# Kernel optimization log

Measured on AMD Instinct MI355X. Metric: run time of the kernel, lower is better.

## Reference

```python
import jax, jax.numpy as jnp
import numpy as np

EMBED = 1024
HIDDEN = 4 * EMBED
EPS = 1e-5

def _layer_norm(x, g, b):
    mu = jnp.mean(x, axis=-1, keepdims=True)
    var = jnp.mean((x - mu) ** 2, axis=-1, keepdims=True)
    return (x - mu) * jax.lax.rsqrt(var + EPS) * g + b

def setup_inputs() -> dict:
    key = jax.random.key(0)
    ks = jax.random.split(key, 8)
    s = 1.0 / np.sqrt(EMBED)
    inp = {
        "x": jax.random.normal(ks[0], (4, 2048, EMBED), dtype=jnp.float32),
        "Wq": jax.random.normal(ks[1], (EMBED, EMBED), dtype=jnp.float32) * s,
        "bq": jnp.zeros((EMBED,), jnp.float32),
        "Wk": jax.random.normal(ks[2], (EMBED, EMBED), dtype=jnp.float32) * s,
        "bk": jnp.zeros((EMBED,), jnp.float32),
        "Wv": jax.random.normal(ks[3], (EMBED, EMBED), dtype=jnp.float32) * s,
        "bv": jnp.zeros((EMBED,), jnp.float32),
        "W1": jax.random.normal(ks[4], (EMBED, HIDDEN), dtype=jnp.float32) * s,
        "b1": jnp.zeros((HIDDEN,), jnp.float32),
        "W2": jax.random.normal(ks[5], (HIDDEN, EMBED), dtype=jnp.float32) * (1.0 / np.sqrt(HIDDEN)),
        "b2": jnp.zeros((EMBED,), jnp.float32),
        "g1": jnp.ones((EMBED,), jnp.float32),
        "be1": jnp.zeros((EMBED,), jnp.float32),
        "g2": jnp.ones((EMBED,), jnp.float32),
        "be2": jnp.zeros((EMBED,), jnp.float32),
    }
    return inp

def reference(x, Wq, bq, Wk, bk, Wv, bv, W1, b1, W2, b2, g1, be1, g2, be2):
    # pre-norm attention
    h = _layer_norm(x, g1, be1)
    Q = h @ Wq + bq  # [B,S,D]
    K = h @ Wk + bk
    V = h @ Wv + bv
    scale = 1.0 / jnp.sqrt(jnp.asarray(EMBED, x.dtype))
    scores = jnp.einsum('bqd,bkd->bqk', Q, K) * scale  # [B,S,S]
    weights = jax.nn.softmax(scores, axis=-1)
    attn = jnp.einsum('bqk,bkd->bqd', weights, V)
    x = x + attn
    # pre-norm MLP
    h2 = _layer_norm(x, g2, be2)
    ff = jax.nn.relu(h2 @ W1 + b1) @ W2 + b2
    return x + ff
```

## Files before the change

### kernel.cpp

```cpp
#include <hip/hip_runtime.h>

#define EMBED 1024
#define HID   4096
#define NB    4
#define SEQ   2048

typedef __attribute__((ext_vector_type(8)))  __bf16 bf16x8;
typedef __attribute__((ext_vector_type(4)))  float  f32x4;
typedef __attribute__((ext_vector_type(4)))  int    i32x4;
typedef unsigned short u16;

__device__ __forceinline__ u16 f2bf(float f) {
  unsigned u = __float_as_uint(f);
  u += 0x7FFFu + ((u >> 16) & 1u);
  return (u16)(u >> 16);
}
__device__ __forceinline__ float bf2f(u16 u) {
  return __uint_as_float(((unsigned)u) << 16);
}

typedef const __attribute__((address_space(1))) unsigned int* gas_t;
typedef __attribute__((address_space(3))) unsigned int* las_t;
__device__ __forceinline__ void gld16(const void* g, void* l) {
  __builtin_amdgcn_global_load_lds((gas_t)g, (las_t)l, 16, 0, 0);
}

#define RD16(p)       __builtin_bit_cast(bf16x8, *(const i32x4*)(p))
#define MFMA16(a,b,c) __builtin_amdgcn_mfma_f32_16x16x32_bf16(a, b, c, 0, 0, 0)
#define SCHED0()      __builtin_amdgcn_sched_barrier(0)
#define BARR()        __builtin_amdgcn_s_barrier()
#define VMW(n)        asm volatile("s_waitcnt vmcnt(" #n ")" ::: "memory")

template<int EPI>
__global__ __launch_bounds__(512, 2) void gemm256v3(
    const u16* __restrict__ A, int lda, long long astr,
    const u16* __restrict__ B, int ldb, long long bstr,
    void* __restrict__ C, int ldc, long long cstr,
    const float* __restrict__ bias,
    float scale, int Kdim)
{
  __shared__ char lds[131072];

  const int tid  = threadIdx.x;
  const int lane = tid & 63;
  const int w    = tid >> 6;
  const int wr   = w >> 2, wc = w & 3;
  const int l15  = lane & 15, l4 = lane >> 4;

  const int gx   = gridDim.x;
  const int nwg  = gx * gridDim.y;
  const int orig = blockIdx.y * gx + blockIdx.x;
  const int t    = ((nwg & 7) == 0) ? ((orig & 7) * (nwg >> 3) + (orig >> 3)) : orig;
  const int bx   = t % gx, by = t / gx;

  const u16* Ab = A + (size_t)blockIdx.z * astr + (size_t)by * 256 * lda;
  const u16* Bb = B + (size_t)blockIdx.z * bstr + (size_t)bx * 256 * ldb;

  const int    srow = tid >> 3;
  const size_t sa   = (size_t)srow * lda + (size_t)(((tid & 7) ^ (srow & 7)) * 8);
  const size_t sb   = (size_t)srow * ldb + (size_t)(((tid & 7) ^ (srow & 7)) * 8);
  const int    ldst = tid * 16;

  auto stA = [&](int buf, int q, int kk) {
    gld16(Ab + (size_t)(q * 64) * lda + kk + sa, lds + buf * 65536 + q * 8192 + ldst);
  };
  auto stB = [&](int buf, int i, int kk) {
    gld16(Bb + (size_t)(i * 64) * ldb + kk + sb, lds + buf * 65536 + 32768 + i * 8192 + ldst);
  };

  const int arow = (wr * 128 + l15) * 128;
  const int brow = 32768 + (wc * 64 + l15) * 128;
  const int cp0  = ((0 + l4) ^ (l15 & 7)) * 16;
  const int cp1  = ((4 + l4) ^ (l15 & 7)) * 16;

  f32x4 acc[8][4] = {};
  const int NT = Kdim >> 6;

  stB(0, 0, 0); stB(0, 1, 0); stB(0, 2, 0); stB(0, 3, 0);
  stA(0, 0, 0); stA(0, 1, 0); stA(0, 2, 0); stA(0, 3, 0);

  for (int T = 0; T < NT; ++T) {
    const char* LB = lds + (T & 1) * 65536;
    VMW(0);
    SCHED0();
    BARR();
    SCHED0();

    if (T + 1 < NT) {
      const int b = (T & 1) ^ 1, kk = (T + 1) * 64;
      stB(b, 0, kk); stB(b, 1, kk); stB(b, 2, kk); stB(b, 3, kk);
      stA(b, 0, kk); stA(b, 1, kk); stA(b, 2, kk); stA(b, 3, kk);
    }

    bf16x8 b0 = RD16(LB + brow + 0 * 2048 + cp0);
    bf16x8 b1 = RD16(LB + brow + 1 * 2048 + cp0);
    bf16x8 b2 = RD16(LB + brow + 2 * 2048 + cp0);
    bf16x8 b3 = RD16(LB + brow + 3 * 2048 + cp0);
    bf16x8 b4 = RD16(LB + brow + 0 * 2048 + cp1);
    bf16x8 b5 = RD16(LB + brow + 1 * 2048 + cp1);
    bf16x8 b6 = RD16(LB + brow + 2 * 2048 + cp1);
    bf16x8 b7 = RD16(LB + brow + 3 * 2048 + cp1);

#define AQ(MP, x0, x1, x2, x3) \
    bf16x8 x0 = RD16(LB + arow + (MP) * 4096 + cp0); \
    bf16x8 x1 = RD16(LB + arow + (MP) * 4096 + cp1); \
    bf16x8 x2 = RD16(LB + arow + (MP) * 4096 + 2048 + cp0); \
    bf16x8 x3 = RD16(LB + arow + (MP) * 4096 + 2048 + cp1);

#define MQ(MP, x0, x1, x2, x3) \
    acc[2*(MP)  ][0] = MFMA16(x0, b0, acc[2*(MP)  ][0]); \
    acc[2*(MP)  ][1] = MFMA16(x0, b1, acc[2*(MP)  ][1]); \
    acc[2*(MP)  ][2] = MFMA16(x0, b2, acc[2*(MP)  ][2]); \
    acc[2*(MP)  ][3] = MFMA16(x0, b3, acc[2*(MP)  ][3]); \
    acc[2*(MP)+1][0] = MFMA16(x2, b0, acc[2*(MP)+1][0]); \
    acc[2*(MP)+1][1] = MFMA16(x2, b1, acc[2*(MP)+1][1]); \
    acc[2*(MP)+1][2] = MFMA16(x2, b2, acc[2*(MP)+1][2]); \
    acc[2*(MP)+1][3] = MFMA16(x2, b3, acc[2*(MP)+1][3]); \
    acc[2*(MP)  ][0] = MFMA16(x1, b4, acc[2*(MP)  ][0]); \
    acc[2*(MP)  ][1] = MFMA16(x1, b5, acc[2*(MP)  ][1]); \
    acc[2*(MP)  ][2] = MFMA16(x1, b6, acc[2*(MP)  ][2]); \
    acc[2*(MP)  ][3] = MFMA16(x1, b7, acc[2*(MP)  ][3]); \
    acc[2*(MP)+1][0] = MFMA16(x3, b4, acc[2*(MP)+1][0]); \
    acc[2*(MP)+1][1] = MFMA16(x3, b5, acc[2*(MP)+1][1]); \
    acc[2*(MP)+1][2] = MFMA16(x3, b6, acc[2*(MP)+1][2]); \
    acc[2*(MP)+1][3] = MFMA16(x3, b7, acc[2*(MP)+1][3]);

    AQ(0, a00, a01, a02, a03)
    AQ(1, a10, a11, a12, a13)
    MQ(0, a00, a01, a02, a03)
    AQ(2, a20, a21, a22, a23)
    MQ(1, a10, a11, a12, a13)
    AQ(3, a30, a31, a32, a33)
    MQ(2, a20, a21, a22, a23)
    MQ(3, a30, a31, a32, a33)
#undef AQ
#undef MQ
  }

  const int bm0 = by * 256 + wr * 128;
  const int bn0 = bx * 256 + wc * 64;
  u16* Ch = (u16*)C;
  #pragma unroll
  for (int mi = 0; mi < 8; ++mi) {
    #pragma unroll
    for (int ni = 0; ni < 4; ++ni) {
      const int col = bn0 + ni * 16 + l15;
      const int r0  = bm0 + mi * 16 + l4 * 4;
      float bv = 0.f;
      if (EPI == 0 || EPI == 3) bv = bias[col];
      #pragma unroll
      for (int r = 0; r < 4; ++r) {
        const size_t idx = (size_t)blockIdx.z * cstr + (size_t)(r0 + r) * ldc + col;
        const float v = acc[mi][ni][r];
        if      (EPI == 0) Ch[idx] = f2bf(v + bv);
        else if (EPI == 3) Ch[idx] = f2bf(fmaxf(v + bv, 0.f));
        else if (EPI == 6) Ch[idx] = f2bf(v * scale);
      }
    }
  }
}

template<int EPI>
__global__ __launch_bounds__(512, 2) void gemm128v3(
    const u16* __restrict__ A, int lda, long long astr,
    const u16* __restrict__ B, int ldb, long long bstr,
    void* __restrict__ C, int ldc, long long cstr,
    const float* __restrict__ bias,
    const void* __restrict__ add,
    float scale, int Kdim)
{
  __shared__ char lds[147456];
  const int SLOT = 49152;

  const int tid  = threadIdx.x;
  const int lane = tid & 63;
  const int w    = tid >> 6;
  const int wr   = w >> 1, wc = w & 1;
  const int l15  = lane & 15, l4 = lane >> 4;

  const int gx   = gridDim.x;
  const int nwg  = gx * gridDim.y;
  const int orig = blockIdx.y * gx + blockIdx.x;
  const int t    = ((nwg & 7) == 0) ? ((orig & 7) * (nwg >> 3) + (orig >> 3)) : orig;
  const int bx   = t % gx, by = t / gx;

  const u16* Ab = A + (size_t)blockIdx.z * astr + (size_t)by * 256 * lda;
  const u16* Bb = B + (size_t)blockIdx.z * bstr + (size_t)bx * 128 * ldb;

  size_t gaoff[4], gboff[2];
  #pragma unroll
  for (int i = 0; i < 4; ++i) {
    const int idx = i * 512 + tid, row = idx >> 3, gc = (idx & 7) ^ (row & 7);
    gaoff[i] = (size_t)row * lda + gc * 8;
  }
  #pragma unroll
  for (int j = 0; j < 2; ++j) {
    const int idx = j * 512 + tid, row = idx >> 3, gc = (idx & 7) ^ (row & 7);
    gboff[j] = (size_t)row * ldb + gc * 8;
  }

  auto stage = [&](char* SB, int kk) {
    #pragma unroll
    for (int i = 0; i < 4; ++i) gld16(Ab + gaoff[i] + kk, SB + (i * 512 + w * 64) * 16);
    #pragma unroll
    for (int j = 0; j < 2; ++j) gld16(Bb + gboff[j] + kk, SB + 32768 + (j * 512 + w * 64) * 16);
  };

  int aoff[4], boff[4];
  #pragma unroll
  for (int m = 0; m < 4; ++m) aoff[m] = (wr * 64 + m * 16 + l15) * 128;
  #pragma unroll
  for (int n = 0; n < 4; ++n) boff[n] = 32768 + (wc * 64 + n * 16 + l15) * 128;
  const int cp0 = ((0 + l4) ^ (l15 & 7)) * 16;
  const int cp1 = ((4 + l4) ^ (l15 & 7)) * 16;

  f32x4 acc[4][4] = {};
  const int NT = Kdim >> 6;

  stage(lds, 0);
  stage(lds + SLOT, 64);

  int sr = 0;
  for (int T = 0; T < NT; ++T) {
    const char* LB = lds + sr * SLOT;
    if (T == NT - 1) VMW(0);
    else             VMW(6);
    SCHED0();
    BARR();
    SCHED0();

    if (T + 2 < NT) stage(lds + ((sr + 2 >= 3) ? sr - 1 : sr + 2) * SLOT, (T + 2) * 64);

    bf16x8 b00 = RD16(LB + boff[0] + cp0);
    bf16x8 b01 = RD16(LB + boff[1] + cp0);
    bf16x8 b02 = RD16(LB + boff[2] + cp0);
    bf16x8 b03 = RD16(LB + boff[3] + cp0);
    bf16x8 b10 = RD16(LB + boff[0] + cp1);
    bf16x8 b11 = RD16(LB + boff[1] + cp1);
    bf16x8 b12 = RD16(LB + boff[2] + cp1);
    bf16x8 b13 = RD16(LB + boff[3] + cp1);
    bf16x8 a00 = RD16(LB + aoff[0] + cp0);
    bf16x8 a10 = RD16(LB + aoff[1] + cp0);
    bf16x8 a20 = RD16(LB + aoff[2] + cp0);
    bf16x8 a30 = RD16(LB + aoff[3] + cp0);
    bf16x8 a01 = RD16(LB + aoff[0] + cp1);
    bf16x8 a11 = RD16(LB + aoff[1] + cp1);
    bf16x8 a21 = RD16(LB + aoff[2] + cp1);
    bf16x8 a31 = RD16(LB + aoff[3] + cp1);

    acc[0][0] = MFMA16(a00, b00, acc[0][0]);
    acc[0][1] = MFMA16(a00, b01, acc[0][1]);
    acc[0][2] = MFMA16(a00, b02, acc[0][2]);
    acc[0][3] = MFMA16(a00, b03, acc[0][3]);
    acc[1][0] = MFMA16(a10, b00, acc[1][0]);
    acc[1][1] = MFMA16(a10, b01, acc[1][1]);
    acc[1][2] = MFMA16(a10, b02, acc[1][2]);
    acc[1][3] = MFMA16(a10, b03, acc[1][3]);
    acc[2][0] = MFMA16(a20, b00, acc[2][0]);
    acc[2][1] = MFMA16(a20, b01, acc[2][1]);
    acc[2][2] = MFMA16(a20, b02, acc[2][2]);
    acc[2][3] = MFMA16(a20, b03, acc[2][3]);
    acc[3][0] = MFMA16(a30, b00, acc[3][0]);
    acc[3][1] = MFMA16(a30, b01, acc[3][1]);
    acc[3][2] = MFMA16(a30, b02, acc[3][2]);
    acc[3][3] = MFMA16(a30, b03, acc[3][3]);
    acc[0][0] = MFMA16(a01, b10, acc[0][0]);
    acc[0][1] = MFMA16(a01, b11, acc[0][1]);
    acc[0][2] = MFMA16(a01, b12, acc[0][2]);
    acc[0][3] = MFMA16(a01, b13, acc[0][3]);
    acc[1][0] = MFMA16(a11, b10, acc[1][0]);
    acc[1][1] = MFMA16(a11, b11, acc[1][1]);
    acc[1][2] = MFMA16(a11, b12, acc[1][2]);
    acc[1][3] = MFMA16(a11, b13, acc[1][3]);
    acc[2][0] = MFMA16(a21, b10, acc[2][0]);
    acc[2][1] = MFMA16(a21, b11, acc[2][1]);
    acc[2][2] = MFMA16(a21, b12, acc[2][2]);
    acc[2][3] = MFMA16(a21, b13, acc[2][3]);
    acc[3][0] = MFMA16(a31, b10, acc[3][0]);
    acc[3][1] = MFMA16(a31, b11, acc[3][1]);
    acc[3][2] = MFMA16(a31, b12, acc[3][2]);
    acc[3][3] = MFMA16(a31, b13, acc[3][3]);

    sr = (sr + 1 == 3) ? 0 : sr + 1;
  }

  const int bm0 = by * 256 + wr * 64;
  const int bn0 = bx * 128 + wc * 64;
  float* Cf = (float*)C;
  u16*   Ch = (u16*)C;
  const float* addf = (const float*)add;
  const u16*   addh = (const u16*)add;
  #pragma unroll
  for (int mi = 0; mi < 4; ++mi) {
    #pragma unroll
    for (int ni = 0; ni < 4; ++ni) {
      const int col = bn0 + ni * 16 + l15;
      const int r0  = bm0 + mi * 16 + l4 * 4;
      float bv = 0.f;
      if (EPI == 8) bv = bias[col];
      #pragma unroll
      for (int r = 0; r < 4; ++r) {
        const size_t idx = (size_t)blockIdx.z * cstr + (size_t)(r0 + r) * ldc + col;
        const float v = acc[mi][ni][r];
        if      (EPI == 5) Ch[idx] = f2bf(v + bias[r0 + r]);
        else if (EPI == 7) Ch[idx] = f2bf(v + addf[idx]);
        else if (EPI == 8) Cf[idx] = v + bv + bf2f(addh[idx]);
      }
    }
  }
}

__global__ __launch_bounds__(256) void ln_kernel(
    const float* __restrict__ x, const float* __restrict__ g,
    const float* __restrict__ be, u16* __restrict__ out)
{
  const int row = blockIdx.x;
  const int tid = threadIdx.x;
  const float4 v = ((const float4*)(x + (size_t)row * EMBED))[tid];
  float s  = v.x + v.y + v.z + v.w;
  float s2 = v.x * v.x + v.y * v.y + v.z * v.z + v.w * v.w;
  #pragma unroll
  for (int m = 1; m < 64; m <<= 1) { s += __shfl_xor(s, m); s2 += __shfl_xor(s2, m); }
  __shared__ float ls[4], ls2[4];
  const int w = tid >> 6;
  if ((tid & 63) == 0) { ls[w] = s; ls2[w] = s2; }
  __syncthreads();
  s  = ls[0] + ls[1] + ls[2] + ls[3];
  s2 = ls2[0] + ls2[1] + ls2[2] + ls2[3];
  const float mu   = s * (1.f / EMBED);
  const float var  = s2 * (1.f / EMBED) - mu * mu;
  const float rstd = rsqrtf(var + 1e-5f);
  const float4 gv = ((const float4*)g)[tid];
  const float4 bv = ((const float4*)be)[tid];
  ushort4 o;
  o.x = f2bf((v.x - mu) * rstd * gv.x + bv.x);
  o.y = f2bf((v.y - mu) * rstd * gv.y + bv.y);
  o.z = f2bf((v.z - mu) * rstd * gv.z + bv.z);
  o.w = f2bf((v.w - mu) * rstd * gv.w + bv.w);
  ((ushort4*)(out + (size_t)row * EMBED))[tid] = o;
}

__global__ __launch_bounds__(256) void ln_bf16(
    const u16* __restrict__ x, const float* __restrict__ g,
    const float* __restrict__ be, u16* __restrict__ out)
{
  const int row = blockIdx.x;
  const int tid = threadIdx.x;
  const ushort4 u = ((const ushort4*)(x + (size_t)row * EMBED))[tid];
  float v0 = bf2f(u.x), v1 = bf2f(u.y), v2 = bf2f(u.z), v3 = bf2f(u.w);
  float s  = v0 + v1 + v2 + v3;
  float s2 = v0 * v0 + v1 * v1 + v2 * v2 + v3 * v3;
  #pragma unroll
  for (int m = 1; m < 64; m <<= 1) { s += __shfl_xor(s, m); s2 += __shfl_xor(s2, m); }
  __shared__ float ls[4], ls2[4];
  const int w = tid >> 6;
  if ((tid & 63) == 0) { ls[w] = s; ls2[w] = s2; }
  __syncthreads();
  s  = ls[0] + ls[1] + ls[2] + ls[3];
  s2 = ls2[0] + ls2[1] + ls2[2] + ls2[3];
  const float mu   = s * (1.f / EMBED);
  const float var  = s2 * (1.f / EMBED) - mu * mu;
  const float rstd = rsqrtf(var + 1e-5f);
  const float4 gv = ((const float4*)g)[tid];
  const float4 bv = ((const float4*)be)[tid];
  ushort4 o;
  o.x = f2bf((v0 - mu) * rstd * gv.x + bv.x);
  o.y = f2bf((v1 - mu) * rstd * gv.y + bv.y);
  o.z = f2bf((v2 - mu) * rstd * gv.z + bv.z);
  o.w = f2bf((v3 - mu) * rstd * gv.w + bv.w);
  ((ushort4*)(out + (size_t)row * EMBED))[tid] = o;
}

__global__ __launch_bounds__(256) void softmax_bf16(
    const u16* __restrict__ S, u16* __restrict__ P)
{
  const int tid = threadIdx.x;
  const size_t base = ((size_t)blockIdx.y * SEQ + blockIdx.x) * SEQ;
  const ushort4* src = (const ushort4*)(S + base);
  const ushort4 ua = src[tid];
  const ushort4 ub = src[tid + 256];
  float a0 = bf2f(ua.x), a1 = bf2f(ua.y), a2 = bf2f(ua.z), a3 = bf2f(ua.w);
  float b0 = bf2f(ub.x), b1 = bf2f(ub.y), b2 = bf2f(ub.z), b3 = bf2f(ub.w);
  float m = fmaxf(fmaxf(fmaxf(a0, a1), fmaxf(a2, a3)),
                  fmaxf(fmaxf(b0, b1), fmaxf(b2, b3)));
  #pragma unroll
  for (int msk = 1; msk < 64; msk <<= 1) m = fmaxf(m, __shfl_xor(m, msk));
  __shared__ float red[8];
  const int w = tid >> 6;
  if ((tid & 63) == 0) red[w] = m;
  __syncthreads();
  m = fmaxf(fmaxf(red[0], red[1]), fmaxf(red[2], red[3]));
  a0 = __expf(a0 - m); a1 = __expf(a1 - m); a2 = __expf(a2 - m); a3 = __expf(a3 - m);
  b0 = __expf(b0 - m); b1 = __expf(b1 - m); b2 = __expf(b2 - m); b3 = __expf(b3 - m);
  float s = a0 + a1 + a2 + a3 + b0 + b1 + b2 + b3;
  #pragma unroll
  for (int msk = 1; msk < 64; msk <<= 1) s += __shfl_xor(s, msk);
  if ((tid & 63) == 0) red[4 + w] = s;
  __syncthreads();
  s = red[4] + red[5] + red[6] + red[7];
  const float inv = 1.0f / s;
  ushort4 oa, ob;
  oa.x = f2bf(a0 * inv); oa.y = f2bf(a1 * inv); oa.z = f2bf(a2 * inv); oa.w = f2bf(a3 * inv);
  ob.x = f2bf(b0 * inv); ob.y = f2bf(b1 * inv); ob.z = f2bf(b2 * inv); ob.w = f2bf(b3 * inv);
  ushort4* dst = (ushort4*)(P + base);
  dst[tid]       = oa;
  dst[tid + 256] = ob;
}

__global__ void transpose_cast3(const float* __restrict__ W0,
                                const float* __restrict__ W1_,
                                const float* __restrict__ W2_,
                                u16* __restrict__ Wt)
{
  __shared__ float t[32][33];
  const int z = blockIdx.z;
  const float* W = (z == 0) ? W0 : (z == 1) ? W1_ : W2_;
  u16* dst = Wt + (size_t)z * EMBED * EMBED;
  const int tx = threadIdx.x, ty = threadIdx.y;
  const int n0 = blockIdx.x * 32, k0 = blockIdx.y * 32;
  #pragma unroll
  for (int i = 0; i < 4; ++i)
    t[ty + i * 8][tx] = W[(size_t)(k0 + ty + i * 8) * EMBED + n0 + tx];
  __syncthreads();
  #pragma unroll
  for (int i = 0; i < 4; ++i)
    dst[(size_t)(n0 + ty + i * 8) * EMBED + k0 + tx] = f2bf(t[tx][ty + i * 8]);
}

__global__ void transpose_cast_f32(const float* __restrict__ W, u16* __restrict__ Wt,
                                   int K, int N)
{
  __shared__ float t[32][33];
  const int tx = threadIdx.x, ty = threadIdx.y;
  const int n0 = blockIdx.x * 32, k0 = blockIdx.y * 32;
  #pragma unroll
  for (int i = 0; i < 4; ++i)
    t[ty + i * 8][tx] = W[(size_t)(k0 + ty + i * 8) * N + n0 + tx];
  __syncthreads();
  #pragma unroll
  for (int i = 0; i < 4; ++i)
    Wt[(size_t)(n0 + ty + i * 8) * K + k0 + tx] = f2bf(t[tx][ty + i * 8]);
}

__global__ void concat_bias2(const float* __restrict__ a, const float* __restrict__ b,
                             float* __restrict__ o)
{
  const int i = blockIdx.x * 1024 + threadIdx.x;
  o[i] = (i < 1024) ? a[i] : b[i - 1024];
}

extern "C" void kernel_launch(void* const* d_in, const int* in_sizes, int n_in,
                              void* d_out, int out_size, void* d_ws, size_t ws_size,
                              hipStream_t stream)
{
  const float* x   = (const float*)d_in[0];
  const float* Wq  = (const float*)d_in[1];
  const float* bq  = (const float*)d_in[2];
  const float* Wk  = (const float*)d_in[3];
  const float* bk  = (const float*)d_in[4];
  const float* Wv  = (const float*)d_in[5];
  const float* bv  = (const float*)d_in[6];
  const float* W1  = (const float*)d_in[7];
  const float* b1  = (const float*)d_in[8];
  const float* W2  = (const float*)d_in[9];
  const float* b2  = (const float*)d_in[10];
  const float* g1  = (const float*)d_in[11];
  const float* be1 = (const float*)d_in[12];
  const float* g2  = (const float*)d_in[13];
  const float* be2 = (const float*)d_in[14];
  float* out = (float*)d_out;

  const size_t RD = (size_t)NB * SEQ * EMBED;

  char* base = (char*)d_ws;
  size_t o = 0;
  auto alloc = [&](size_t bytes) -> void* {
    o = (o + 255) & ~(size_t)255;
    void* p = base + o;
    o += bytes;
    return p;
  };

  u16*   wqkv3T = (u16*)alloc((size_t)3 * EMBED * EMBED * 2);
  u16*   w1T    = (u16*)alloc((size_t)HID * EMBED * 2);
  u16*   w2T    = (u16*)alloc((size_t)EMBED * HID * 2);
  float* bqk    = (float*)alloc(2048 * 4);
  u16*   h      = (u16*)alloc(RD * 2);
  u16*   QKb    = (u16*)alloc(RD * 2 * 2);
  u16*   Vt     = (u16*)alloc(RD * 2);
  u16*   x2     = (u16*)alloc(RD * 2);

  const size_t need_batched = o + (size_t)NB * SEQ * SEQ * 4 + 1024;
  const int NZ = (ws_size >= need_batched) ? NB : 1;
  u16* Sb16 = (u16*)alloc((size_t)NZ * SEQ * SEQ * 2);
  u16* Pb   = (u16*)alloc((size_t)NZ * SEQ * SEQ * 2);
  u16* ff   = (NZ == NB) ? Sb16
                         : (u16*)alloc((size_t)NB * SEQ * HID * 2);

  const u16* wqkT = wqkv3T;
  const u16* wvT  = wqkv3T + (size_t)2 * EMBED * EMBED;

  const dim3 blk(512);
  const dim3 tblk(32, 8);

  transpose_cast3<<<dim3(32, 32, 3), tblk, 0, stream>>>(Wq, Wk, Wv, wqkv3T);
  transpose_cast_f32<<<dim3(HID / 32, EMBED / 32), tblk, 0, stream>>>(W1, w1T, EMBED, HID);
  transpose_cast_f32<<<dim3(EMBED / 32, HID / 32), tblk, 0, stream>>>(W2, w2T, HID, EMBED);
  concat_bias2<<<dim3(2), dim3(1024), 0, stream>>>(bq, bk, bqk);

  ln_kernel<<<dim3(NB * SEQ), dim3(256), 0, stream>>>(x, g1, be1, h);

  gemm256v3<0><<<dim3(2048 / 256, NB * SEQ / 256, 1), blk, 0, stream>>>(
      h, EMBED, 0LL, wqkT, EMBED, 0LL, QKb, 2048, 0LL, bqk, 1.f, EMBED);

  gemm128v3<5><<<dim3(SEQ / 128, EMBED / 256, NB), blk, 0, stream>>>(
      wvT, EMBED, 0LL, h, EMBED, (long long)SEQ * EMBED,
      Vt, SEQ, (long long)EMBED * SEQ, bv, nullptr, 1.f, EMBED);

  for (int b = 0; b < NB; b += NZ) {
    const u16* Qp  = QKb + (size_t)b * SEQ * 2048;
    const u16* Kp  = Qp + 1024;
    const u16* Vtp = Vt + (size_t)b * EMBED * SEQ;
    u16* x2p       = x2 + (size_t)b * SEQ * EMBED;
    const float* xp = x + (size_t)b * SEQ * EMBED;
    gemm256v3<6><<<dim3(SEQ / 256, SEQ / 256, NZ), blk, 0, stream>>>(
        Qp, 2048, (long long)SEQ * 2048, Kp, 2048, (long long)SEQ * 2048,
        Sb16, SEQ, (long long)SEQ * SEQ, nullptr, 0.03125f, EMBED);
    softmax_bf16<<<dim3(SEQ, NZ), dim3(256), 0, stream>>>(Sb16, Pb);
    gemm128v3<7><<<dim3(EMBED / 128, SEQ / 256, NZ), blk, 0, stream>>>(
        Pb, SEQ, (long long)SEQ * SEQ, Vtp, SEQ, (long long)EMBED * SEQ,
        x2p, EMBED, (long long)SEQ * EMBED, nullptr, xp, 1.f, SEQ);
  }

  ln_bf16<<<dim3(NB * SEQ), dim3(256), 0, stream>>>(x2, g2, be2, h);

  gemm256v3<3><<<dim3(HID / 256, NB * SEQ / 256, 1), blk, 0, stream>>>(
      h, EMBED, 0LL, w1T, EMBED, 0LL, ff, HID, 0LL, b1, 1.f, EMBED);
  gemm128v3<8><<<dim3(EMBED / 128, NB * SEQ / 256, 1), blk, 0, stream>>>(
      ff, HID, 0LL, w2T, HID, 0LL, out, EMBED, 0LL, b2, x2, 1.f, HID);
}
```

Measured before the change: 316.3 us.

## Add 4-wave 256x256 GEMM kernel with 128x128 per-wave tiles for MLP up-projection

Introduces a new GEMM kernel using 256 threads (4 waves), each computing a 128x128 sub-tile with 64 accumulator fragments. It double-buffers 64-deep K tiles in LDS and swizzles block order for L2 locality. The W1 GEMM now uses this kernel instead of the 8-wave 256x256 kernel, which cuts LDS reads per MFMA. In exchange, the large accumulator set needs many registers and allows only one block per CU, which may reduce latency hiding.

After: 334.8 us. 5.8% more time.

```diff
diff --git a/kernel.cpp b/kernel.cpp
--- a/kernel.cpp
+++ b/kernel.cpp
@@ -30,6 +30,147 @@
 #define SCHED0()      __builtin_amdgcn_sched_barrier(0)
 #define BARR()        __builtin_amdgcn_s_barrier()
 #define VMW(n)        asm volatile("s_waitcnt vmcnt(" #n ")" ::: "memory")
+
+template<int EPI>
+__global__ __launch_bounds__(256, 1) void gemmw4(
+    const u16* __restrict__ A, int lda, long long astr,
+    const u16* __restrict__ B, int ldb, long long bstr,
+    void* __restrict__ C, int ldc, long long cstr,
+    const float* __restrict__ bias,
+    float scale, int Kdim)
+{
+  __shared__ char lds[131072];
+
+  const int tid  = threadIdx.x;
+  const int lane = tid & 63;
+  const int w    = tid >> 6;
+  const int wr   = w >> 1, wc = w & 1;
+  const int l15  = lane & 15, l4 = lane >> 4;
+
+  const int gx   = gridDim.x;
+  const int nwg  = gx * gridDim.y;
+  const int orig = blockIdx.y * gx + blockIdx.x;
+  const int t    = ((nwg & 7) == 0) ? ((orig & 7) * (nwg >> 3) + (orig >> 3)) : orig;
+  const int bx   = t % gx, by = t / gx;
+
+  const u16* Ab = A + (size_t)blockIdx.z * astr + (size_t)by * 256 * lda;
+  const u16* Bb = B + (size_t)blockIdx.z * bstr + (size_t)bx * 256 * ldb;
+
+  const int    srow = tid >> 3;
+  const int    sch  = (tid & 7) ^ (srow & 7);
+  const size_t sa   = (size_t)srow * lda + sch * 8;
+  const size_t sb   = (size_t)srow * ldb + sch * 8;
+
+  auto stage = [&](char* SB, int kk) {
+    #pragma unroll
+    for (int u = 0; u < 8; ++u)
+      gld16(Ab + (size_t)(u * 32) * lda + kk + sa, SB + u * 4096 + tid * 16);
+    #pragma unroll
+    for (int u = 0; u < 8; ++u)
+      gld16(Bb + (size_t)(u * 32) * ldb + kk + sb, SB + 32768 + u * 4096 + tid * 16);
+  };
+
+  const int arow = (wr * 128 + l15) * 128;
+  const int brow = 32768 + (wc * 128 + l15) * 128;
+  const int cp0  = ((0 + l4) ^ (l15 & 7)) * 16;
+  const int cp1  = ((4 + l4) ^ (l15 & 7)) * 16;
+
+  f32x4 acc[8][8] = {};
+  const int NT = Kdim >> 6;
+
+  stage(lds, 0);
+
+  for (int T = 0; T < NT; ++T) {
+    const char* LB = lds + (T & 1) * 65536;
+    VMW(0);
+    SCHED0();
+    BARR();
+    SCHED0();
+
+    if (T + 1 < NT) stage(lds + ((T & 1) ^ 1) * 65536, (T + 1) * 64);
+
+    bf16x8 p0 = RD16(LB + brow + 0 * 2048 + cp0);
+    bf16x8 p1 = RD16(LB + brow + 1 * 2048 + cp0);
+    bf16x8 p2 = RD16(LB + brow + 2 * 2048 + cp0);
+    bf16x8 p3 = RD16(LB + brow + 3 * 2048 + cp0);
+    bf16x8 p4 = RD16(LB + brow + 4 * 2048 + cp0);
+    bf16x8 p5 = RD16(LB + brow + 5 * 2048 + cp0);
+    bf16x8 p6 = RD16(LB + brow + 6 * 2048 + cp0);
+    bf16x8 p7 = RD16(LB + brow + 7 * 2048 + cp0);
+    bf16x8 u0 = RD16(LB + arow + 0 * 2048 + cp0);
+    bf16x8 u1 = RD16(LB + arow + 1 * 2048 + cp0);
+    bf16x8 u2 = RD16(LB + arow + 2 * 2048 + cp0);
+    bf16x8 u3 = RD16(LB + arow + 3 * 2048 + cp0);
+    bf16x8 u4 = RD16(LB + arow + 4 * 2048 + cp0);
+    bf16x8 u5 = RD16(LB + arow + 5 * 2048 + cp0);
+    bf16x8 u6 = RD16(LB + arow + 6 * 2048 + cp0);
+    bf16x8 u7 = RD16(LB + arow + 7 * 2048 + cp0);
+    bf16x8 q0 = RD16(LB + brow + 0 * 2048 + cp1);
+    bf16x8 q1 = RD16(LB + brow + 1 * 2048 + cp1);
+    bf16x8 q2 = RD16(LB + brow + 2 * 2048 + cp1);
+    bf16x8 q3 = RD16(LB + brow + 3 * 2048 + cp1);
+    bf16x8 q4 = RD16(LB + brow + 4 * 2048 + cp1);
+    bf16x8 q5 = RD16(LB + brow + 5 * 2048 + cp1);
+    bf16x8 q6 = RD16(LB + brow + 6 * 2048 + cp1);
+    bf16x8 q7 = RD16(LB + brow + 7 * 2048 + cp1);
+    bf16x8 v0 = RD16(LB + arow + 0 * 2048 + cp1);
+    bf16x8 v1 = RD16(LB + arow + 1 * 2048 + cp1);
+    bf16x8 v2 = RD16(LB + arow + 2 * 2048 + cp1);
+    bf16x8 v3 = RD16(LB + arow + 3 * 2048 + cp1);
+    bf16x8 v4 = RD16(LB + arow + 4 * 2048 + cp1);
+    bf16x8 v5 = RD16(LB + arow + 5 * 2048 + cp1);
+    bf16x8 v6 = RD16(LB + arow + 6 * 2048 + cp1);
+    bf16x8 v7 = RD16(LB + arow + 7 * 2048 + cp1);
+
+#define MROW(MI, AF) \
+    acc[MI][0] = MFMA16(AF, p0, acc[MI][0]); \
+    acc[MI][1] = MFMA16(AF, p1, acc[MI][1]); \
+    acc[MI][2] = MFMA16(AF, p2, acc[MI][2]); \
+    acc[MI][3] = MFMA16(AF, p3, acc[MI][3]); \
+    acc[MI][4] = MFMA16(AF, p4, acc[MI][4]); \
+    acc[MI][5] = MFMA16(AF, p5, acc[MI][5]); \
+    acc[MI][6] = MFMA16(AF, p6, acc[MI][6]); \
+    acc[MI][7] = MFMA16(AF, p7, acc[MI][7]);
+#define NROW(MI, AF) \
+    acc[MI][0] = MFMA16(AF, q0, acc[MI][0]); \
+    acc[MI][1] = MFMA16(AF, q1, acc[MI][1]); \
+    acc[MI][2] = MFMA16(AF, q2, acc[MI][2]); \
+    acc[MI][3] = MFMA16(AF, q3, acc[MI][3]); \
+    acc[MI][4] = MFMA16(AF, q4, acc[MI][4]); \
+    acc[MI][5] = MFMA16(AF, q5, acc[MI][5]); \
+    acc[MI][6] = MFMA16(AF, q6, acc[MI][6]); \
+    acc[MI][7] = MFMA16(AF, q7, acc[MI][7]);
+
+    MROW(0, u0) MROW(1, u1) MROW(2, u2) MROW(3, u3)
+    MROW(4, u4) MROW(5, u5) MROW(6, u6) MROW(7, u7)
+    NROW(0, v0) NROW(1, v1) NROW(2, v2) NROW(3, v3)
+    NROW(4, v4) NROW(5, v5) NROW(6, v6) NROW(7, v7)
+#undef MROW
+#undef NROW
+  }
+
+  const int bm0 = by * 256 + wr * 128;
+  const int bn0 = bx * 256 + wc * 128;
+  u16* Ch = (u16*)C;
+  #pragma unroll
+  for (int mi = 0; mi < 8; ++mi) {
+    #pragma unroll
+    for (int ni = 0; ni < 8; ++ni) {
+      const int col = bn0 + ni * 16 + l15;
+      const int r0  = bm0 + mi * 16 + l4 * 4;
+      float bv = 0.f;
+      if (EPI == 0 || EPI == 3) bv = bias[col];
+      #pragma unroll
+      for (int r = 0; r < 4; ++r) {
+        const size_t idx = (size_t)blockIdx.z * cstr + (size_t)(r0 + r) * ldc + col;
+        const float v = acc[mi][ni][r];
+        if      (EPI == 0) Ch[idx] = f2bf(v + bv);
+        else if (EPI == 3) Ch[idx] = f2bf(fmaxf(v + bv, 0.f));
+        else if (EPI == 6) Ch[idx] = f2bf(v * scale);
+      }
+    }
+  }
+}
 
 template<int EPI>
 __global__ __launch_bounds__(512, 2) void gemm256v3(
@@ -534,7 +675,7 @@
 
   ln_bf16<<<dim3(NB * SEQ), dim3(256), 0, stream>>>(x2, g2, be2, h);
 
-  gemm256v3<3><<<dim3(HID / 256, NB * SEQ / 256, 1), blk, 0, stream>>>(
+  gemmw4<3><<<dim3(HID / 256, NB * SEQ / 256, 1), dim3(256), 0, stream>>>(
       h, EMBED, 0LL, w1T, EMBED, 0LL, ff, HID, 0LL, b1, 1.f, EMBED);
   gemm128v3<8><<<dim3(EMBED / 128, NB * SEQ / 256, 1), blk, 0, stream>>>(
       ff, HID, 0LL, w2T, HID, 0LL, out, EMBED, 0LL, b2, x2, 1.f, HID);
```
